# Kernel tuning notes

Hardware: AMD Instinct MI355X
Metric: run time of the kernel (lower is better)

## Reference

```python
import jax, jax.numpy as jnp
import numpy as np

ALPHA = 0.5
TEMP = 0.1
BIG = 1.0e10
THRESH = 1.0e9
NEG = -1.0e10


def setup_inputs() -> dict:
    key = jax.random.key(0)
    k1, k2, k3, k4, k5 = jax.random.split(key, 5)
    B, T, N = 2, 4, 4096
    pred_positions = jax.random.normal(k1, (B, T, N, 3), dtype=jnp.float32)
    target_positions = jax.random.normal(k2, (B, T, N, 3), dtype=jnp.float32)
    is_controller = jax.random.bernoulli(k3, 0.1, (B, N))
    padding_mask = jax.random.bernoulli(k4, 0.95, (B, N))           # True = valid
    visibility_mask = jax.random.bernoulli(k5, 0.9, (B, T, N))      # True = visible
    return {
        "pred_positions": pred_positions,
        "target_positions": target_positions,
        "is_controller": is_controller,
        "padding_mask": padding_mask,
        "visibility_mask": visibility_mask,
    }


def _soft_max(x, temp):
    # differentiable max: sum(x * softmax(x / temp)) with all-invalid rows -> 0
    valid = x > -THRESH
    has_valid = valid.any(axis=-1)
    w = jax.nn.softmax(x / temp, axis=-1)
    r = (x * w).sum(axis=-1)
    return jnp.where(has_valid, r, jnp.zeros_like(r))


def _hybrid_loss(pred, target, mask, alpha, temp):
    # pred, target: (B, T, N, 3); mask: (B, T, N) bool (same mask for pred & target)
    xx = (pred ** 2).sum(-1)[..., :, None]          # (B,T,N,1)
    yy = (target ** 2).sum(-1)[..., None, :]        # (B,T,1,M)
    xy = jnp.einsum('btnd,btmd->btnm', pred, target)
    dist = jnp.maximum(xx + yy - 2.0 * xy, 0.0)     # (B,T,N,M) squared distances

    tgt_m = mask[..., None, :]                      # mask over target axis
    prd_m = mask[..., :, None]                      # mask over pred axis

    d_for_pred = jnp.where(tgt_m, dist, BIG)
    min_p = d_for_pred.min(axis=-1)                 # (B,T,N) min over targets
    d_for_tgt = jnp.where(prd_m, dist, BIG)
    min_t = d_for_tgt.min(axis=-2)                  # (B,T,M) min over preds

    # --- Chamfer ---
    maskf = mask.astype(pred.dtype)
    cd_p = jnp.where(min_p > THRESH, 0.0, min_p) * maskf
    cd_t = jnp.where(min_t > THRESH, 0.0, min_t) * maskf
    num_valid = jnp.maximum(maskf.sum(-1), 1.0)     # (B,T)
    cd = cd_p.sum(-1) / num_valid + cd_t.sum(-1) / num_valid

    # --- Soft Hausdorff ---
    hp = jnp.where(mask, jnp.minimum(min_p, THRESH), NEG)
    ht = jnp.where(mask, jnp.minimum(min_t, THRESH), NEG)
    hd = jnp.maximum(_soft_max(hp, temp), _soft_max(ht, temp))

    cd_loss = cd.mean()                             # mean over (B,T) == per-step mean then /T
    hd_loss = hd.mean()
    total = alpha * cd_loss + (1.0 - alpha) * hd_loss
    return total, cd_loss, hd_loss


def reference(pred_positions, target_positions, is_controller, padding_mask, visibility_mask):
    # object_only=True: particle_mask = ~is_controller & padding_mask
    particle_mask = (~is_controller) & padding_mask          # (B,N)
    mask = particle_mask[:, None, :] & visibility_mask       # (B,T,N)
    total, cd, hd = _hybrid_loss(pred_positions, target_positions, mask, ALPHA, TEMP)
    return total
```

## Files before the change

kernel.cpp:

```cpp
#include <hip/hip_runtime.h>

#define NB 2
#define NT 4
#define NN 4096
#define NBT (NB*NT)
#define TOTAL (NBT*NN)
#define BIGF 1e10f
#define THRESHF 1e9f
#define NEGF (-1e10f)

typedef __attribute__((ext_vector_type(8)))  short s16x8;
typedef __attribute__((ext_vector_type(16))) float f32x16;

__device__ inline unsigned short f2bf(float f) {
    unsigned u = __float_as_uint(f);
    u += 0x7fffu + ((u >> 16) & 1u);
    return (unsigned short)(u >> 16);
}
__device__ inline void split2(float x, unsigned short& hi, unsigned short& lo) {
    hi = f2bf(x);
    float fh = __uint_as_float(((unsigned)hi) << 16);
    lo = f2bf(x - fh);
}
__device__ inline s16x8 mk8(unsigned short a, unsigned short b, unsigned short c, unsigned short d,
                            unsigned short e, unsigned short f, unsigned short g, unsigned short h) {
    return (s16x8){(short)a,(short)b,(short)c,(short)d,(short)e,(short)f,(short)g,(short)h};
}


__global__ __launch_bounds__(256, 2) void min_kernel(
    const float* __restrict__ pred, const float* __restrict__ targ,
    const int* __restrict__ ic, const int* __restrict__ pad, const int* __restrict__ vis,
    unsigned* __restrict__ minp, unsigned* __restrict__ mint,
    float* __restrict__ out)
{
    __shared__ s16x8 ldsB[4096];
    const int tid  = threadIdx.x;
    const int lane = tid & 63;
    const int w    = tid >> 6;
    const int cc   = blockIdx.x;
    const int rc   = blockIdx.y;
    const int z    = blockIdx.z;
    const int bt   = z >> 1;
    const int dir  = z & 1;
    const int b    = bt >> 2;
    if (cc == 0 && rc == 0 && z == 0 && tid == 0) out[0] = 0.0f;

    const float* __restrict__ rowraw = dir ? targ : pred;
    const float* __restrict__ colraw = dir ? pred : targ;
    unsigned* outp = (dir ? mint : minp) + cc * TOTAL;
    const unsigned short one = 0x3F80;

    #pragma unroll
    for (int r = 0; r < 8; ++r) {
        int nloc = r*256 + tid;
        int n    = cc*2048 + nloc;
        int gi   = bt*NN + n;
        bool m = (ic[b*NN + n] == 0) && (pad[b*NN + n] != 0) && (vis[gi] != 0);
        float bias = m ? 0.0f : BIGF;
        float x = colraw[3*gi], y = colraw[3*gi+1], zc = colraw[3*gi+2];
        unsigned short ux,uy,uz,vx,vy,vz,ch,cl;
        split2(-2.0f*x,ux,vx); split2(-2.0f*y,uy,vy); split2(-2.0f*zc,uz,vz);
        float wn = fmaf(x,x, fmaf(y,y, zc*zc));
        split2(wn + bias, ch, cl);
        int tile = nloc >> 5;
        int c32  = tid & 31;
        ldsB[tile*64 + c32]      = mk8(ux,uy,uz,ux,uy,uz,vx,vy);
        ldsB[tile*64 + 32 + c32] = mk8(vz,ch,cl,one,one,0,0,0);
    }

    const int h  = lane >> 5;
    const int c  = lane & 31;
    const int n0 = rc*256 + w*64;
    s16x8 a[2];
    #pragma unroll
    for (int rt = 0; rt < 2; ++rt) {
        int row = bt*NN + n0 + rt*32 + c;
        float x = rowraw[3*row], y = rowraw[3*row+1], zc = rowraw[3*row+2];
        unsigned short ax,ay,az,bx,by,bz,wh,wl;
        split2(x,ax,bx); split2(y,ay,by); split2(zc,az,bz);
        float wn = fmaf(x,x, fmaf(y,y, zc*zc));
        split2(wn, wh, wl);
        a[rt] = h ? mk8(az,one,one,wh,wl,0,0,0) : mk8(ax,ay,az,bx,by,bz,ax,ay);
    }

    __syncthreads();

    f32x16 zf, mm[2];
    #pragma unroll
    for (int q = 0; q < 16; ++q) { zf[q] = 0.0f; mm[0][q] = 3.4e38f; mm[1][q] = 3.4e38f; }

    #pragma unroll 1
    for (int tp = 0; tp < 32; ++tp) {
        s16x8 b0 = ldsB[tp*128 + lane];
        s16x8 b1 = ldsB[tp*128 + 64 + lane];
        #pragma unroll
        for (int rt = 0; rt < 2; ++rt) {
            f32x16 D0 = __builtin_amdgcn_mfma_f32_32x32x16_bf16(a[rt], b0, zf, 0, 0, 0);
            f32x16 D1 = __builtin_amdgcn_mfma_f32_32x32x16_bf16(a[rt], b1, zf, 0, 0, 0);
            #pragma unroll
            for (int q = 0; q < 16; ++q)
                mm[rt][q] = fminf(fminf(D0[q], D1[q]), mm[rt][q]);
        }
    }

    #pragma unroll
    for (int off = 1; off <= 16; off <<= 1) {
        #pragma unroll
        for (int rt = 0; rt < 2; ++rt) {
            #pragma unroll
            for (int q = 0; q < 16; ++q)
                mm[rt][q] = fminf(mm[rt][q], __shfl_xor(mm[rt][q], off));
        }
    }

    #pragma unroll
    for (int j = 0; j < 16; ++j) {
        if (c == j) {
            const int ro = (j & 3) + 8*(j >> 2) + 4*h;
            const int rb = bt*NN + n0 + ro;
            #pragma unroll
            for (int rt = 0; rt < 2; ++rt) {
                float x = mm[rt][j];
                unsigned bits = __float_as_uint(fmaxf(x, 0.0f));
                if (!(x == x))           bits = __float_as_uint(BIGF);
                if (bits == 0x80000000u) bits = 0u;
                outp[rb + rt*32] = bits;
            }
        }
    }
}

__global__ __launch_bounds__(1024) void finalize_kernel(
    const unsigned* __restrict__ minp, const unsigned* __restrict__ mint,
    const int* __restrict__ ic, const int* __restrict__ pad, const int* __restrict__ vis,
    float* __restrict__ out)
{
    const int bt  = blockIdx.x;
    const int b   = bt >> 2;
    const int tid = threadIdx.x;

    uint4 p0 = ((const uint4*)(minp + bt*NN))[tid];
    uint4 p1 = ((const uint4*)(minp + TOTAL + bt*NN))[tid];
    uint4 t0 = ((const uint4*)(mint + bt*NN))[tid];
    uint4 t1 = ((const uint4*)(mint + TOTAL + bt*NN))[tid];
    int4 ic4  = ((const int4*)(ic  + b*NN))[tid];
    int4 pad4 = ((const int4*)(pad + b*NN))[tid];
    int4 vis4 = ((const int4*)(vis + bt*NN))[tid];

    unsigned pu[4] = { p0.x < p1.x ? p0.x : p1.x, p0.y < p1.y ? p0.y : p1.y,
                       p0.z < p1.z ? p0.z : p1.z, p0.w < p1.w ? p0.w : p1.w };
    unsigned tu[4] = { t0.x < t1.x ? t0.x : t1.x, t0.y < t1.y ? t0.y : t1.y,
                       t0.z < t1.z ? t0.z : t1.z, t0.w < t1.w ? t0.w : t1.w };
    int icv[4]  = { ic4.x, ic4.y, ic4.z, ic4.w };
    int padv[4] = { pad4.x, pad4.y, pad4.z, pad4.w };
    int visv[4] = { vis4.x, vis4.y, vis4.z, vis4.w };

    float hp[4], ht[4];
    float nv = 0.f, scdp = 0.f, scdt = 0.f, mhp = NEGF, mht = NEGF;
    #pragma unroll
    for (int e = 0; e < 4; ++e) {
        bool m = (icv[e] == 0) && (padv[e] != 0) && (visv[e] != 0);
        float mp = __uint_as_float(pu[e]);
        float mt = __uint_as_float(tu[e]);
        if (!(mp <= 2e10f)) mp = BIGF;
        if (!(mt <= 2e10f)) mt = BIGF;
        float hpv = m ? fminf(mp, THRESHF) : NEGF;
        float htv = m ? fminf(mt, THRESHF) : NEGF;
        hp[e] = hpv; ht[e] = htv;
        if (m) {
            nv += 1.f;
            scdp += (mp > THRESHF) ? 0.f : mp;
            scdt += (mt > THRESHF) ? 0.f : mt;
            mhp = fmaxf(mhp, hpv);
            mht = fmaxf(mht, htv);
        }
    }

    __shared__ float red[16][5];
    const int wid = tid >> 6;
    #pragma unroll
    for (int o = 32; o > 0; o >>= 1) {
        nv   += __shfl_xor(nv, o);
        scdp += __shfl_xor(scdp, o);
        scdt += __shfl_xor(scdt, o);
        mhp   = fmaxf(mhp, __shfl_xor(mhp, o));
        mht   = fmaxf(mht, __shfl_xor(mht, o));
    }
    if ((tid & 63) == 0) {
        red[wid][0] = nv; red[wid][1] = scdp; red[wid][2] = scdt;
        red[wid][3] = mhp; red[wid][4] = mht;
    }
    __syncthreads();
    nv = 0.f; scdp = 0.f; scdt = 0.f; mhp = NEGF; mht = NEGF;
    #pragma unroll
    for (int k = 0; k < 16; ++k) {
        nv += red[k][0]; scdp += red[k][1]; scdt += red[k][2];
        mhp = fmaxf(mhp, red[k][3]); mht = fmaxf(mht, red[k][4]);
    }
    __syncthreads();

    float Zp = 0.f, Sp = 0.f, Zt = 0.f, St = 0.f;
    #pragma unroll
    for (int e = 0; e < 4; ++e) {
        float hpv = hp[e];
        if (hpv > -THRESHF) { float x = __expf((hpv - mhp) * 10.0f); Zp += x; Sp += hpv * x; }
        float htv = ht[e];
        if (htv > -THRESHF) { float x = __expf((htv - mht) * 10.0f); Zt += x; St += htv * x; }
    }
    #pragma unroll
    for (int o = 32; o > 0; o >>= 1) {
        Zp += __shfl_xor(Zp, o);
        Sp += __shfl_xor(Sp, o);
        Zt += __shfl_xor(Zt, o);
        St += __shfl_xor(St, o);
    }
    __shared__ float red2[16][4];
    if ((tid & 63) == 0) {
        red2[wid][0] = Zp; red2[wid][1] = Sp; red2[wid][2] = Zt; red2[wid][3] = St;
    }
    __syncthreads();
    if (tid == 0) {
        Zp = 0.f; Sp = 0.f; Zt = 0.f; St = 0.f;
        #pragma unroll
        for (int k = 0; k < 16; ++k) {
            Zp += red2[k][0]; Sp += red2[k][1]; Zt += red2[k][2]; St += red2[k][3];
        }
        float nvm = fmaxf(nv, 1.f);
        float cd  = scdp / nvm + scdt / nvm;
        float sp  = (nv > 0.f) ? (Sp / Zp) : 0.f;
        float st  = (nv > 0.f) ? (St / Zt) : 0.f;
        float hd  = fmaxf(sp, st);
        atomicAdd(out, (0.5f * cd + 0.5f * hd) * 0.125f);
    }
}

extern "C" void kernel_launch(void* const* d_in, const int* in_sizes, int n_in,
                              void* d_out, int out_size, void* d_ws, size_t ws_size,
                              hipStream_t stream)
{
    const float* pred = (const float*)d_in[0];
    const float* targ = (const float*)d_in[1];
    const int*   ic   = (const int*)d_in[2];
    const int*   pad  = (const int*)d_in[3];
    const int*   vis  = (const int*)d_in[4];
    float* out = (float*)d_out;

    unsigned* minp = (unsigned*)d_ws;
    unsigned* mint = minp + 2*TOTAL;

    dim3 grid(2, 16, 16);
    min_kernel<<<grid, 256, 0, stream>>>(pred, targ, ic, pad, vis, minp, mint, out);
    finalize_kernel<<<NBT, 1024, 0, stream>>>(minp, mint, ic, pad, vis, out);
}
```

Baseline: 27.12 us.

## Split column range four ways and reduce row minima through LDS transpose

The column dimension is split into four chunks instead of two. That doubles the grid to 2048 blocks, halves the per-block LDS tile and loop trip count, and raises the launch-bounds occupancy hint to 4 blocks per CU. The final per-row min reduction now writes the MFMA accumulators into a padded LDS buffer, and each lane reduces one row serially, replacing 5 rounds of cross-lane shuffles and the masked per-lane stores. The finalize kernel reads four partial minima instead of two, which adds extra workspace traffic and more blocks redoing the row-side setup.

```diff
diff --git a/kernel.cpp b/kernel.cpp
--- a/kernel.cpp
+++ b/kernel.cpp
@@ -28,13 +28,15 @@
 }
 
 
-__global__ __launch_bounds__(256, 2) void min_kernel(
+__global__ __launch_bounds__(256, 4) void min_kernel(
     const float* __restrict__ pred, const float* __restrict__ targ,
     const int* __restrict__ ic, const int* __restrict__ pad, const int* __restrict__ vis,
     unsigned* __restrict__ minp, unsigned* __restrict__ mint,
     float* __restrict__ out)
 {
-    __shared__ s16x8 ldsB[4096];
+    __shared__ __align__(16) char ldsraw[33792];
+    s16x8* ldsB = (s16x8*)ldsraw;
+
     const int tid  = threadIdx.x;
     const int lane = tid & 63;
     const int w    = tid >> 6;
@@ -52,9 +54,9 @@
     const unsigned short one = 0x3F80;
 
     #pragma unroll
-    for (int r = 0; r < 8; ++r) {
+    for (int r = 0; r < 4; ++r) {
         int nloc = r*256 + tid;
-        int n    = cc*2048 + nloc;
+        int n    = cc*1024 + nloc;
         int gi   = bt*NN + n;
         bool m = (ic[b*NN + n] == 0) && (pad[b*NN + n] != 0) && (vis[gi] != 0);
         float bias = m ? 0.0f : BIGF;
@@ -91,7 +93,7 @@
     for (int q = 0; q < 16; ++q) { zf[q] = 0.0f; mm[0][q] = 3.4e38f; mm[1][q] = 3.4e38f; }
 
     #pragma unroll 1
-    for (int tp = 0; tp < 32; ++tp) {
+    for (int tp = 0; tp < 16; ++tp) {
         s16x8 b0 = ldsB[tp*128 + lane];
         s16x8 b1 = ldsB[tp*128 + 64 + lane];
         #pragma unroll
@@ -104,31 +106,26 @@
         }
     }
 
-    #pragma unroll
-    for (int off = 1; off <= 16; off <<= 1) {
+    __syncthreads();
+    float* fbuf = (float*)ldsraw;
+    const int wbase = w * 2112;
+    #pragma unroll
+    for (int rt = 0; rt < 2; ++rt) {
         #pragma unroll
-        for (int rt = 0; rt < 2; ++rt) {
-            #pragma unroll
-            for (int q = 0; q < 16; ++q)
-                mm[rt][q] = fminf(mm[rt][q], __shfl_xor(mm[rt][q], off));
-        }
-    }
-
-    #pragma unroll
-    for (int j = 0; j < 16; ++j) {
-        if (c == j) {
-            const int ro = (j & 3) + 8*(j >> 2) + 4*h;
-            const int rb = bt*NN + n0 + ro;
-            #pragma unroll
-            for (int rt = 0; rt < 2; ++rt) {
-                float x = mm[rt][j];
-                unsigned bits = __float_as_uint(fmaxf(x, 0.0f));
-                if (!(x == x))           bits = __float_as_uint(BIGF);
-                if (bits == 0x80000000u) bits = 0u;
-                outp[rb + rt*32] = bits;
-            }
-        }
-    }
+        for (int q = 0; q < 16; ++q) {
+            int rl = rt*32 + (q & 3) + 8*(q >> 2) + 4*h;
+            fbuf[wbase + rl*33 + c] = mm[rt][q];
+        }
+    }
+    const float* rowp = fbuf + wbase + lane*33;
+    float v = 3.4e38f;
+    #pragma unroll
+    for (int k = 0; k < 32; ++k) v = fminf(v, rowp[k]);
+    float xv = fmaxf(v, 0.0f);
+    unsigned bits = __float_as_uint(xv);
+    if (!(xv == xv))         bits = __float_as_uint(BIGF);
+    if (bits == 0x80000000u) bits = 0u;
+    outp[bt*NN + n0 + lane] = bits;
 }
 
 __global__ __launch_bounds__(1024) void finalize_kernel(
@@ -139,19 +136,22 @@
     const int bt  = blockIdx.x;
     const int b   = bt >> 2;
     const int tid = threadIdx.x;
-
-    uint4 p0 = ((const uint4*)(minp + bt*NN))[tid];
-    uint4 p1 = ((const uint4*)(minp + TOTAL + bt*NN))[tid];
-    uint4 t0 = ((const uint4*)(mint + bt*NN))[tid];
-    uint4 t1 = ((const uint4*)(mint + TOTAL + bt*NN))[tid];
+    const int S   = TOTAL/4;
+
+    const uint4* pp = (const uint4*)(minp + bt*NN);
+    const uint4* tt = (const uint4*)(mint + bt*NN);
+    uint4 p0 = pp[tid], p1 = pp[S + tid], p2 = pp[2*S + tid], p3 = pp[3*S + tid];
+    uint4 t0 = tt[tid], t1 = tt[S + tid], t2 = tt[2*S + tid], t3 = tt[3*S + tid];
     int4 ic4  = ((const int4*)(ic  + b*NN))[tid];
     int4 pad4 = ((const int4*)(pad + b*NN))[tid];
     int4 vis4 = ((const int4*)(vis + bt*NN))[tid];
 
-    unsigned pu[4] = { p0.x < p1.x ? p0.x : p1.x, p0.y < p1.y ? p0.y : p1.y,
-                       p0.z < p1.z ? p0.z : p1.z, p0.w < p1.w ? p0.w : p1.w };
-    unsigned tu[4] = { t0.x < t1.x ? t0.x : t1.x, t0.y < t1.y ? t0.y : t1.y,
-                       t0.z < t1.z ? t0.z : t1.z, t0.w < t1.w ? t0.w : t1.w };
+    #define MIN4(a,b,c,d) min(min(a,b), min(c,d))
+    unsigned pu[4] = { MIN4(p0.x,p1.x,p2.x,p3.x), MIN4(p0.y,p1.y,p2.y,p3.y),
+                       MIN4(p0.z,p1.z,p2.z,p3.z), MIN4(p0.w,p1.w,p2.w,p3.w) };
+    unsigned tu[4] = { MIN4(t0.x,t1.x,t2.x,t3.x), MIN4(t0.y,t1.y,t2.y,t3.y),
+                       MIN4(t0.z,t1.z,t2.z,t3.z), MIN4(t0.w,t1.w,t2.w,t3.w) };
+    #undef MIN4
     int icv[4]  = { ic4.x, ic4.y, ic4.z, ic4.w };
     int padv[4] = { pad4.x, pad4.y, pad4.z, pad4.w };
     int visv[4] = { vis4.x, vis4.y, vis4.z, vis4.w };
@@ -247,9 +247,9 @@
     float* out = (float*)d_out;
 
     unsigned* minp = (unsigned*)d_ws;
-    unsigned* mint = minp + 2*TOTAL;
-
-    dim3 grid(2, 16, 16);
+    unsigned* mint = minp + 4*TOTAL;
+
+    dim3 grid(4, 16, 16);
     min_kernel<<<grid, 256, 0, stream>>>(pred, targ, ic, pad, vis, minp, mint, out);
     finalize_kernel<<<NBT, 1024, 0, stream>>>(minp, mint, ic, pad, vis, out);
 }
```

Result: faster. 23.56 us (-13.1%).
